# Performance work log

Hardware: AMD Instinct MI355X
Metric: run time of the kernel (lower is better)

The kernel has to match this reference:

```python
import jax, jax.numpy as jnp
import numpy as np

FILTER_LENGTH = 1024
HOP_LENGTH = 512
CUTOFF = FILTER_LENGTH // 2 + 1  # 513
PAD = FILTER_LENGTH // 2


def _make_forward_basis():
    # Real/imag DFT basis, rows = [Re(0..cutoff-1); Im(0..cutoff-1)], cols = time taps
    fb = np.fft.fft(np.eye(FILTER_LENGTH))
    basis = np.vstack([np.real(fb[:CUTOFF, :]), np.imag(fb[:CUTOFF, :])]).astype(np.float32)
    # periodic ('fftbins') Hann window, win_length == filter_length so no centering pad
    n = np.arange(FILTER_LENGTH)
    window = (0.5 - 0.5 * np.cos(2.0 * np.pi * n / FILTER_LENGTH)).astype(np.float32)
    return jnp.asarray(basis * window[None, :])  # [1026, 1024]


def setup_inputs() -> dict:
    key = jax.random.key(0)
    input_data = jax.random.normal(key, (16, 1048576), dtype=jnp.float32)
    forward_basis = _make_forward_basis()
    return {"input_data": input_data, "forward_basis": forward_basis}


def reference(input_data, forward_basis):
    # reflect-pad, frame, windowed DFT via conv1d, then magnitude
    x = jnp.pad(input_data, ((0, 0), (PAD, PAD)), mode="reflect")[:, None, :]  # [B,1,L+1024]
    y = jax.lax.conv_general_dilated(
        x,
        forward_basis[:, None, :],  # [1026, 1, 1024]
        window_strides=(HOP_LENGTH,),
        padding="VALID",
        dimension_numbers=("NCH", "OIH", "NCH"),
    )  # [B, 1026, T]
    real = y[:, :CUTOFF, :]
    imag = y[:, CUTOFF:, :]
    return jnp.sqrt(real * real + imag * imag)  # [B, 513, T]
```

## Files before the change

kernel.cpp:

```cpp
#include <hip/hip_runtime.h>
#include <math.h>

#define L_IN   1048576
#define NBATCH 16
#define T_FR   2049
#define NBINS  513

struct C2 { float r, i; };
__device__ __forceinline__ C2 cadd(C2 a, C2 b){ return {a.r+b.r, a.i+b.i}; }
__device__ __forceinline__ C2 csub(C2 a, C2 b){ return {a.r-b.r, a.i-b.i}; }
__device__ __forceinline__ C2 cmul(C2 a, C2 b){ return {a.r*b.r - a.i*b.i, a.r*b.i + a.i*b.r}; }
__device__ __forceinline__ C2 cnegi(C2 a){ return {a.i, -a.r}; }
#define RSQ2 0.70710678118654752f
__device__ __forceinline__ C2 cw8 (C2 a){ return { RSQ2*(a.r+a.i),  RSQ2*(a.i-a.r)}; }
__device__ __forceinline__ C2 cw83(C2 a){ return { RSQ2*(a.i-a.r), -RSQ2*(a.r+a.i)}; }

#if __has_builtin(__builtin_amdgcn_sqrtf)
#define FSQRT(x) __builtin_amdgcn_sqrtf(x)
#else
#define FSQRT(x) sqrtf(x)
#endif

__device__ __forceinline__ void dft8(const C2 x[8], C2 y[8]) {
  C2 ea0 = cadd(x[0], x[4]), ea1 = csub(x[0], x[4]);
  C2 eb0 = cadd(x[2], x[6]), eb1 = csub(x[2], x[6]);
  C2 oa0 = cadd(x[1], x[5]), oa1 = csub(x[1], x[5]);
  C2 ob0 = cadd(x[3], x[7]), ob1 = csub(x[3], x[7]);
  C2 E0 = cadd(ea0, eb0), E2 = csub(ea0, eb0);
  C2 nb = cnegi(eb1);
  C2 E1 = cadd(ea1, nb),  E3 = csub(ea1, nb);
  C2 O0 = cadd(oa0, ob0), O2 = csub(oa0, ob0);
  C2 no = cnegi(ob1);
  C2 O1 = cadd(oa1, no),  O3 = csub(oa1, no);
  y[0] = cadd(E0, O0);  y[4] = csub(E0, O0);
  C2 t1 = cw8(O1);      y[1] = cadd(E1, t1); y[5] = csub(E1, t1);
  C2 t2 = cnegi(O2);    y[2] = cadd(E2, t2); y[6] = csub(E2, t2);
  C2 t3 = cw83(O3);     y[3] = cadd(E3, t3); y[7] = csub(E3, t3);
}

__device__ __forceinline__ int phys(int idx) { return idx ^ ((idx >> 4) & 15); }

__device__ __forceinline__ unsigned short f2bf(float f) {
  unsigned int u = __builtin_bit_cast(unsigned int, f);
  u += 0x7FFFu + ((u >> 16) & 1u);
  return (unsigned short)(u >> 16);
}

#define TWOPI 6.283185307179586f

__device__ __forceinline__ void load_raw(float2 v[8], const float* __restrict__ xb,
                                         int tt, int t) {
  const int s0 = tt*512 - 512;
  if (tt != 0 && tt != 2048) {
    #pragma unroll
    for (int j = 0; j < 8; ++j) v[j] = *(const float2*)&xb[s0 + 2*(t + 64*j)];
  } else {
    #pragma unroll
    for (int j = 0; j < 8; ++j) {
      int e0 = s0 + 2*(t + 64*j), e1 = e0 + 1;
      int r0 = e0 < 0 ? -e0 : (e0 >= L_IN ? 2*L_IN - 2 - e0 : e0);
      int r1 = e1 < 0 ? -e1 : (e1 >= L_IN ? 2*L_IN - 2 - e1 : e1);
      v[j] = { xb[r0], xb[r1] };
    }
  }
}

__device__ __forceinline__ void process_frame(const float2 v[8], const float2 wl[8],
    const C2 tws1[8], const C2 tws2[8], const C2 vu[4],
    C2* __restrict__ cfw, unsigned short (* __restrict__ mag)[18], int t, int tl)
{
  C2 x[8], y[8];
  #pragma unroll
  for (int j = 0; j < 8; ++j) x[j] = { v[j].x * wl[j].x, v[j].y * wl[j].y };
  dft8(x, y);
  #pragma unroll
  for (int k = 0; k < 8; ++k) cfw[phys(8*t + k)] = y[k];
  {
    const int m = t & 7, g = t >> 3;
    C2 xs[8];
    #pragma unroll
    for (int j = 0; j < 8; ++j) xs[j] = cfw[phys(t + 64*j)];
    #pragma unroll
    for (int j = 1; j < 8; ++j) xs[j] = cmul(xs[j], tws1[j]);
    dft8(xs, y);
    #pragma unroll
    for (int k = 0; k < 8; ++k) cfw[phys(g*64 + m + 8*k)] = y[k];
  }
  C2 z[8];
  {
    C2 xs[8];
    #pragma unroll
    for (int j = 0; j < 8; ++j) xs[j] = cfw[phys(t + 64*j)];
    #pragma unroll
    for (int j = 1; j < 8; ++j) xs[j] = cmul(xs[j], tws2[j]);
    dft8(xs, z);
  }
  const int pl = (64 - t) & 63;
  #pragma unroll
  for (int j = 0; j < 4; ++j) {
    const int k = t + 64*j;
    C2 Zp = { __shfl(z[7-j].r, pl), __shfl(z[7-j].i, pl) };
    if (t == 0) Zp = z[(8-j) & 7];
    C2 Zk = z[j];
    C2 V  = vu[j];
    float Are = Zk.r + Zp.r, Aim = Zk.i - Zp.i;
    float Bre = Zk.r - Zp.r, Bim = Zk.i + Zp.i;
    float VBr = V.r*Bre - V.i*Bim;
    float VBi = V.r*Bim + V.i*Bre;
    float Xr = Are + VBr, Xi = Aim + VBi;
    float Yr = Are - VBr, Yi = Aim - VBi;
    mag[k][tl]       = f2bf(FSQRT(Xr*Xr + Xi*Xi));
    mag[512 - k][tl] = f2bf(FSQRT(Yr*Yr + Yi*Yi));
  }
  if (t == 0) {
    C2 z4 = z[4];
    mag[256][tl] = f2bf(2.0f * FSQRT(z4.r*z4.r + z4.i*z4.i));
  }
}

__global__ __launch_bounds__(256, 3)
void stft_fft(const float* __restrict__ input,
              const float* __restrict__ basis,
              float* __restrict__ out)
{
  __shared__ C2 cf[4][512];
  __shared__ unsigned short mag[513][18];

  const int tid = threadIdx.x;
  const int t   = tid & 63;
  const int w   = tid >> 6;
  const int b   = blockIdx.y;
  const int t0  = blockIdx.x << 4;

  C2 tws1[8], tws2[8], vu[4];
  {
    const float SN[4] = {0.f, 0.3826834324f, 0.7071067812f, 0.9238795325f};
    const float CS[4] = {1.f, 0.9238795325f, 0.7071067812f, 0.3826834324f};
    float s, c;
    __sincosf((TWOPI/64.0f)   * (float)(t & 7), &s, &c); C2 W1 = { c, -s };
    __sincosf((TWOPI/512.0f)  * (float)t,       &s, &c); C2 W2 = { c, -s };
    __sincosf((TWOPI/1024.0f) * (float)t,       &s, &c); C2 Wt = { c, -s };
    tws1[1] = W1;  tws2[1] = W2;
    #pragma unroll
    for (int j = 2; j < 8; ++j) {
      tws1[j] = cmul(tws1[j-1], W1);
      tws2[j] = cmul(tws2[j-1], W2);
    }
    #pragma unroll
    for (int j = 0; j < 4; ++j) {
      C2 D = { -SN[j], -CS[j] };
      vu[j] = cmul(Wt, D);
    }
  }

  float2 wl[8];
  #pragma unroll
  for (int j = 0; j < 8; ++j) {
    float2 wv = *(const float2*)&basis[2*(t + 64*j)];
    wl[j] = { 0.5f * wv.x, 0.5f * wv.y };
  }

  const float* xb = input + (size_t)b * L_IN;
  C2* cfw = cf[w];
  const int base = t0 + w*4;

  float2 v0[8], v1[8];
  if (base     <= 2048) load_raw(v0, xb, base,     t);
  if (base + 1 <= 2048) load_raw(v1, xb, base + 1, t);
  if (base     <= 2048) process_frame(v0, wl, tws1, tws2, vu, cfw, mag, t, w*4);
  if (base + 2 <= 2048) load_raw(v0, xb, base + 2, t);
  if (base + 1 <= 2048) process_frame(v1, wl, tws1, tws2, vu, cfw, mag, t, w*4 + 1);
  if (base + 3 <= 2048) load_raw(v1, xb, base + 3, t);
  if (base + 2 <= 2048) process_frame(v0, wl, tws1, tws2, vu, cfw, mag, t, w*4 + 2);
  if (base + 3 <= 2048) process_frame(v1, wl, tws1, tws2, vu, cfw, mag, t, w*4 + 3);

  __syncthreads();

  const size_t ob = (size_t)b * NBINS * T_FR;
  for (int idx = tid; idx < NBINS*16; idx += 256) {
    const int row = idx >> 4, tl = idx & 15, tt = t0 + tl;
    if (tt <= 2048) {
      unsigned int u = (unsigned int)mag[row][tl] << 16;
      out[ob + (size_t)row * T_FR + tt] = __builtin_bit_cast(float, u);
    }
  }
}

extern "C" void kernel_launch(void* const* d_in, const int* in_sizes, int n_in,
                              void* d_out, int out_size, void* d_ws, size_t ws_size,
                              hipStream_t stream) {
  const float* input = (const float*)d_in[0];
  const float* basis = (const float*)d_in[1];
  float* out = (float*)d_out;
  stft_fft<<<dim3(129, 16), 256, 0, stream>>>(input, basis, out);
}
```

Baseline: 48.38 us.

## Process two 16-frame groups per block with prefetch and packed bf16 LDS staging

Each block now handles 32 frames in two halves, loading the next half's raw input before flushing the first half's magnitudes. Mirrored bin pairs (k and 512-k) are packed into one 32-bit LDS word, which halves the number of LDS stores. Frame indices are clamped rather than branched on, so out-of-range frames recompute frame 2048 and only the writes are masked. The intent is to overlap global loads with the flush and to amortise per-block twiddle and window setup. The cost is half as many blocks (65x16), which lowers parallelism and adds wave-quantisation and barrier overhead.

```diff
diff --git a/kernel.cpp b/kernel.cpp
--- a/kernel.cpp
+++ b/kernel.cpp
@@ -40,10 +40,10 @@
 
 __device__ __forceinline__ int phys(int idx) { return idx ^ ((idx >> 4) & 15); }
 
-__device__ __forceinline__ unsigned short f2bf(float f) {
+__device__ __forceinline__ unsigned int f2bf(float f) {
   unsigned int u = __builtin_bit_cast(unsigned int, f);
   u += 0x7FFFu + ((u >> 16) & 1u);
-  return (unsigned short)(u >> 16);
+  return u >> 16;
 }
 
 #define TWOPI 6.283185307179586f
@@ -67,7 +67,7 @@
 
 __device__ __forceinline__ void process_frame(const float2 v[8], const float2 wl[8],
     const C2 tws1[8], const C2 tws2[8], const C2 vu[4],
-    C2* __restrict__ cfw, unsigned short (* __restrict__ mag)[18], int t, int tl)
+    C2* __restrict__ cfw, unsigned int (* __restrict__ mag2)[19], int t, int tl)
 {
   C2 x[8], y[8];
   #pragma unroll
@@ -109,12 +109,14 @@
     float VBi = V.r*Bim + V.i*Bre;
     float Xr = Are + VBr, Xi = Aim + VBi;
     float Yr = Are - VBr, Yi = Aim - VBi;
-    mag[k][tl]       = f2bf(FSQRT(Xr*Xr + Xi*Xi));
-    mag[512 - k][tl] = f2bf(FSQRT(Yr*Yr + Yi*Yi));
+    float mX = FSQRT(Xr*Xr + Xi*Xi);
+    float mY = FSQRT(Yr*Yr + Yi*Yi);
+    mag2[k][tl] = f2bf(mX) | (f2bf(mY) << 16);
   }
   if (t == 0) {
     C2 z4 = z[4];
-    mag[256][tl] = f2bf(2.0f * FSQRT(z4.r*z4.r + z4.i*z4.i));
+    unsigned int m256 = f2bf(2.0f * FSQRT(z4.r*z4.r + z4.i*z4.i));
+    mag2[256][tl] = m256 | (m256 << 16);
   }
 }
 
@@ -124,13 +126,13 @@
               float* __restrict__ out)
 {
   __shared__ C2 cf[4][512];
-  __shared__ unsigned short mag[513][18];
+  __shared__ unsigned int mag2[257][19];
 
   const int tid = threadIdx.x;
   const int t   = tid & 63;
   const int w   = tid >> 6;
   const int b   = blockIdx.y;
-  const int t0  = blockIdx.x << 4;
+  const int t0  = blockIdx.x << 5;
 
   C2 tws1[8], tws2[8], vu[4];
   {
@@ -162,28 +164,47 @@
 
   const float* xb = input + (size_t)b * L_IN;
   C2* cfw = cf[w];
-  const int base = t0 + w*4;
+  const size_t ob = (size_t)b * NBINS * T_FR;
+  const int bw = t0 + 4*w;
+  const int F0 = bw      < 2048 ? bw      : 2048;
+  const int F1 = bw + 1  < 2048 ? bw + 1  : 2048;
+  const int F2 = bw + 2  < 2048 ? bw + 2  : 2048;
+  const int F3 = bw + 3  < 2048 ? bw + 3  : 2048;
+  const int G0 = bw + 16 < 2048 ? bw + 16 : 2048;
+  const int G1 = bw + 17 < 2048 ? bw + 17 : 2048;
+  const int G2 = bw + 18 < 2048 ? bw + 18 : 2048;
+  const int G3 = bw + 19 < 2048 ? bw + 19 : 2048;
+
+  #define FLUSH(h) do {                                                       \
+    __syncthreads();                                                          \
+    for (int idx = tid; idx < NBINS*16; idx += 256) {                         \
+      const int row = idx >> 4, tl = idx & 15, tt = t0 + (h)*16 + tl;         \
+      if (tt <= 2048) {                                                       \
+        const int s_ = row > 256;                                             \
+        const int p_ = s_ ? 512 - row : row;                                  \
+        unsigned int pk = mag2[p_][tl];                                       \
+        unsigned int u = (s_ ? (pk & 0xFFFF0000u) : (pk << 16));              \
+        out[ob + (size_t)row * T_FR + tt] = __builtin_bit_cast(float, u);     \
+      }                                                                       \
+    }                                                                         \
+    __syncthreads();                                                          \
+  } while (0)
 
   float2 v0[8], v1[8];
-  if (base     <= 2048) load_raw(v0, xb, base,     t);
-  if (base + 1 <= 2048) load_raw(v1, xb, base + 1, t);
-  if (base     <= 2048) process_frame(v0, wl, tws1, tws2, vu, cfw, mag, t, w*4);
-  if (base + 2 <= 2048) load_raw(v0, xb, base + 2, t);
-  if (base + 1 <= 2048) process_frame(v1, wl, tws1, tws2, vu, cfw, mag, t, w*4 + 1);
-  if (base + 3 <= 2048) load_raw(v1, xb, base + 3, t);
-  if (base + 2 <= 2048) process_frame(v0, wl, tws1, tws2, vu, cfw, mag, t, w*4 + 2);
-  if (base + 3 <= 2048) process_frame(v1, wl, tws1, tws2, vu, cfw, mag, t, w*4 + 3);
-
-  __syncthreads();
-
-  const size_t ob = (size_t)b * NBINS * T_FR;
-  for (int idx = tid; idx < NBINS*16; idx += 256) {
-    const int row = idx >> 4, tl = idx & 15, tt = t0 + tl;
-    if (tt <= 2048) {
-      unsigned int u = (unsigned int)mag[row][tl] << 16;
-      out[ob + (size_t)row * T_FR + tt] = __builtin_bit_cast(float, u);
-    }
-  }
+  load_raw(v0, xb, F0, t);
+  load_raw(v1, xb, F1, t);
+  process_frame(v0, wl, tws1, tws2, vu, cfw, mag2, t, 4*w    ); load_raw(v0, xb, F2, t);
+  process_frame(v1, wl, tws1, tws2, vu, cfw, mag2, t, 4*w + 1); load_raw(v1, xb, F3, t);
+  process_frame(v0, wl, tws1, tws2, vu, cfw, mag2, t, 4*w + 2); load_raw(v0, xb, G0, t);
+  process_frame(v1, wl, tws1, tws2, vu, cfw, mag2, t, 4*w + 3); load_raw(v1, xb, G1, t);
+  FLUSH(0);
+  process_frame(v0, wl, tws1, tws2, vu, cfw, mag2, t, 4*w    ); load_raw(v0, xb, G2, t);
+  process_frame(v1, wl, tws1, tws2, vu, cfw, mag2, t, 4*w + 1); load_raw(v1, xb, G3, t);
+  process_frame(v0, wl, tws1, tws2, vu, cfw, mag2, t, 4*w + 2);
+  process_frame(v1, wl, tws1, tws2, vu, cfw, mag2, t, 4*w + 3);
+  FLUSH(1);
+
+  #undef FLUSH
 }
 
 extern "C" void kernel_launch(void* const* d_in, const int* in_sizes, int n_in,
@@ -192,5 +213,5 @@
   const float* input = (const float*)d_in[0];
   const float* basis = (const float*)d_in[1];
   float* out = (float*)d_out;
-  stft_fft<<<dim3(129, 16), 256, 0, stream>>>(input, basis, out);
-}
+  stft_fft<<<dim3(65, 16), 256, 0, stream>>>(input, basis, out);
+}
```

New measurement: 55.01 us. 13.7% more time.
